# Kernel tuning notes

Hardware: AMD Instinct MI355X
Metric: run time of the kernel (lower is better)

Reference implementation:

```python
import jax, jax.numpy as jnp
import numpy as np

N_NODES = 50000
N_EDGES = 800000
MAX_ITER = 20  # torchdeq default f_max_iter=40; fixed iteration count for a tractable jit-able baseline
K = 3          # TAGConv default number of hops
INS, EMB, HID, OUT = 4, 64, 128, 1


def setup_inputs():
    key = jax.random.key(0)
    ks = jax.random.split(key, 12)
    def lin(k, fan_in, fan_out):
        return jax.random.normal(k, (fan_in, fan_out), jnp.float32) / np.sqrt(fan_in)
    def tag_w(k, fan_in, fan_out):
        # stacked weights for the K+1 TAGConv linear maps: [K+1, in, out]
        return jax.random.normal(k, (K + 1, fan_in, fan_out), jnp.float32) / np.sqrt(fan_in * (K + 1))
    return {
        "x": jax.random.normal(ks[0], (N_NODES, INS), jnp.float32),
        "pos": jax.random.normal(ks[1], (N_NODES, 3), jnp.float32),
        "edge_attr": jax.random.uniform(ks[2], (N_EDGES,), jnp.float32),
        "up_w1": lin(ks[3], INS, EMB), "up_b1": jnp.zeros((EMB,), jnp.float32),
        "up_w2": lin(ks[4], EMB, EMB), "up_b2": jnp.zeros((EMB,), jnp.float32),
        "c1_w": tag_w(ks[5], EMB + 3, HID), "c1_b": jnp.zeros((HID,), jnp.float32),
        "c2_w": tag_w(ks[6], HID, HID), "c2_b": jnp.zeros((HID,), jnp.float32),
        "c3_w": tag_w(ks[7], HID, EMB), "c3_b": jnp.zeros((EMB,), jnp.float32),
        "down_w1": lin(ks[8], EMB, OUT), "down_b1": jnp.zeros((OUT,), jnp.float32),
        "down_w2": lin(ks[9], OUT, OUT), "down_b2": jnp.zeros((OUT,), jnp.float32),
        "edge_index": jax.random.randint(ks[10], (2, N_EDGES), 0, N_NODES, jnp.int32),
    }


def _gcn_norm(row, col, edge_attr, n):
    # PyG gcn_norm with edge weights, no self loops (TAGConv default)
    deg = jax.ops.segment_sum(edge_attr, col, num_segments=n)
    safe = jnp.where(deg > 0, deg, 1.0)
    dinv = jnp.where(deg > 0, jax.lax.rsqrt(safe), 0.0)
    return dinv[row] * edge_attr * dinv[col]


def _mlp(x, w1, b1, w2, b2):
    # torch F.gelu default = exact erf gelu
    return jax.nn.gelu(x @ w1 + b1, approximate=False) @ w2 + b2


def reference(x, pos, edge_attr, up_w1, up_b1, up_w2, up_b2, c1_w, c1_b, c2_w, c2_b, c3_w, c3_b, down_w1, down_b1, down_w2, down_b2, edge_index):
    n = x.shape[0]
    row, col = edge_index[0], edge_index[1]
    norm = _gcn_norm(row, col, edge_attr, n)

    def tag(h, W, b):
        # TAGConv: sum_k lin_k( A_hat^k x ) + bias
        out = h @ W[0]
        for k in range(1, W.shape[0]):
            h = jax.ops.segment_sum(h[row] * norm[:, None], col, num_segments=n)  # [E,C] gather-scatter
            out = out + h @ W[k]
        return out + b

    def gnn(z):
        h = jnp.concatenate([z, pos], axis=1)
        h = jax.nn.relu(tag(h, c1_w, c1_b))
        h = jax.nn.relu(tag(h, c2_w, c2_b))  # F.dropout is identity in eval mode
        h = tag(h, c3_w, c3_b)
        return jax.nn.log_softmax(h, axis=1)

    z0 = _mlp(x, up_w1, up_b1, up_w2, up_b2)
    z = jax.lax.fori_loop(0, MAX_ITER, lambda i, zz: gnn(zz), z0)  # fixed-point solver
    z_star = gnn(z)  # phantom-gradient step (torchdeq grad=1)
    out = _mlp(z_star, down_w1, down_b1, down_w2, down_b2)
    return out, z_star
```

## Files before the change

kernel.cpp:

```cpp
#include <hip/hip_runtime.h>
#include <hip/hip_bf16.h>

#define N_NODES 50000
#define N_EDGES 800000
#define MAX_ITER 20

typedef __attribute__((ext_vector_type(8))) short bf16x8;
typedef __attribute__((ext_vector_type(4))) float f32x4;
typedef __attribute__((ext_vector_type(2))) float f32x2;
typedef unsigned char uchar;

__device__ __forceinline__ float gelu_f(float x){
  return 0.5f*x*(1.0f+erff(x*0.70710678118654752f));
}
__device__ __forceinline__ ushort f2b(float f){
  uint x = __float_as_uint(f);
  uint r = (x + 0x7fffu + ((x>>16)&1u)) >> 16;
  return (ushort)r;
}

#if __has_builtin(__builtin_amdgcn_cvt_pk_f32_fp8) && __has_builtin(__builtin_amdgcn_cvt_pk_fp8_f32)
#define HW_FP8 1
#endif

__device__ __forceinline__ uint fp8_enc1_sw(float x){
  uint u = __float_as_uint(x);
  uint s = (u>>24)&0x80u;
  int e = (int)((u>>23)&0xffu);
  uint m = u&0x7fffffu;
  uint m3 = (m + 0x80000u)>>20;
  if (m3==8u){ e+=1; m3=0u; }
  int e8 = e-120;
  if (e8<=0) return s;
  if (e8>=15) return s|0x7eu;
  return s | ((uint)e8<<3) | m3;
}
__device__ __forceinline__ float fp8_dec1_sw(uint b){
  uint s=(b&0x80u)<<24;
  uint em=b&0x7fu;
  if (em==0u) return __uint_as_float(s);
  if ((em>>3)==0u) return (s?-1.f:1.f)*(float)em*0.001953125f;
  return __uint_as_float(s | ((em+960u)<<20));
}
__device__ __forceinline__ void fp8_dec8(uint lo, uint hi, float* d){
#ifdef HW_FP8
  f32x2 a = __builtin_amdgcn_cvt_pk_f32_fp8(lo,false);
  f32x2 b = __builtin_amdgcn_cvt_pk_f32_fp8(lo,true);
  f32x2 c = __builtin_amdgcn_cvt_pk_f32_fp8(hi,false);
  f32x2 e = __builtin_amdgcn_cvt_pk_f32_fp8(hi,true);
  d[0]=a[0];d[1]=a[1];d[2]=b[0];d[3]=b[1];d[4]=c[0];d[5]=c[1];d[6]=e[0];d[7]=e[1];
#else
  d[0]=fp8_dec1_sw(lo&0xffu);        d[1]=fp8_dec1_sw((lo>>8)&0xffu);
  d[2]=fp8_dec1_sw((lo>>16)&0xffu);  d[3]=fp8_dec1_sw(lo>>24);
  d[4]=fp8_dec1_sw(hi&0xffu);        d[5]=fp8_dec1_sw((hi>>8)&0xffu);
  d[6]=fp8_dec1_sw((hi>>16)&0xffu);  d[7]=fp8_dec1_sw(hi>>24);
#endif
}
__device__ __forceinline__ uint fp8_enc4(float a,float b,float c,float d){
#ifdef HW_FP8
  uint u = __builtin_amdgcn_cvt_pk_fp8_f32(a,b,0u,false);
  u = __builtin_amdgcn_cvt_pk_fp8_f32(c,d,u,true);
  return u;
#else
  return fp8_enc1_sw(a) | (fp8_enc1_sw(b)<<8) | (fp8_enc1_sw(c)<<16) | (fp8_enc1_sw(d)<<24);
#endif
}
__device__ __forceinline__ uchar fp8_enc1(float a){
#ifdef HW_FP8
  return (uchar)(__builtin_amdgcn_cvt_pk_fp8_f32(a,a,0u,false)&0xffu);
#else
  return (uchar)fp8_enc1_sw(a);
#endif
}

__global__ void deg_cnt_kernel(const int* __restrict__ col, const float* __restrict__ attr,
                               float* __restrict__ deg, int* __restrict__ cnt){
  int e = blockIdx.x*256 + threadIdx.x;
  if (e < N_EDGES){
    int c = col[e];
    atomicAdd(&deg[c], attr[e]);
    atomicAdd(&cnt[c], 1);
  }
}

__global__ void norm_kernel(const int* __restrict__ row, const int* __restrict__ col,
                            const float* __restrict__ attr, const float* __restrict__ deg,
                            float* __restrict__ nrm){
  int e = blockIdx.x*256 + threadIdx.x;
  if (e < N_EDGES){
    float dr = deg[row[e]], dc = deg[col[e]];
    float ir = dr > 0.f ? rsqrtf(dr) : 0.f;
    float ic = dc > 0.f ? rsqrtf(dc) : 0.f;
    nrm[e] = ir * attr[e] * ic;
  }
}

__global__ void scan_kernel(const int* __restrict__ cnt, int* __restrict__ starts,
                            int* __restrict__ cursor){
  __shared__ int buf[1024];
  __shared__ int carry;
  int tid = threadIdx.x;
  if (tid==0) carry = 0;
  __syncthreads();
  for (int base=0; base<N_NODES; base+=1024){
    int i = base+tid;
    int v = (i<N_NODES)? cnt[i] : 0;
    int cv = carry;
    buf[tid]=v;
    __syncthreads();
    for (int off=1; off<1024; off<<=1){
      int t = (tid>=off)? buf[tid-off] : 0;
      __syncthreads();
      buf[tid]+=t;
      __syncthreads();
    }
    int excl = buf[tid]-v+cv;
    if (i<N_NODES){ starts[i]=excl; cursor[i]=excl; }
    __syncthreads();
    if (tid==0) carry = cv + buf[1023];
    __syncthreads();
  }
  if (tid==0) starts[N_NODES] = carry;
}

__global__ void fill_kernel(const int* __restrict__ row, const int* __restrict__ col,
                            const float* __restrict__ nrm, int* __restrict__ cursor,
                            int* __restrict__ csr_row, float* __restrict__ csr_nrm){
  int e = blockIdx.x*256+threadIdx.x;
  if (e<N_EDGES){
    int c = col[e];
    int p = atomicAdd(&cursor[c],1);
    csr_row[p]=row[e];
    csr_nrm[p]=nrm[e];
  }
}

__global__ void pack_w1(const float* __restrict__ W, ushort* __restrict__ PB){
  int i = blockIdx.x*256+threadIdx.x;
  if (i < 4*8*128*8){
    int e = i&7; int n = (i>>3)&127; int kb = (i>>10)&7; int j = i>>13;
    int k = kb*8+e;
    PB[i] = f2b(W[((size_t)j*67 + k)*128 + n]);
  }
}
__global__ void pack_w2(const float* __restrict__ W, ushort* __restrict__ PB){
  int i = blockIdx.x*256+threadIdx.x;
  if (i < 4*16*128*8){
    int e = i&7; int n = (i>>3)&127; int kb = (i>>10)&15; int j = i>>14;
    int k = kb*8+e;
    PB[i] = f2b(W[((size_t)j*128 + k)*128 + n]);
  }
}
__global__ void pack_w3(const float* __restrict__ W, ushort* __restrict__ PB){
  int i = blockIdx.x*256+threadIdx.x;
  if (i < 16*256*8){
    int e = i&7; int n = (i>>3)&255; int kb = i>>11;
    int k = kb*8+e;
    PB[i] = f2b(W[(((size_t)(n>>6))*128 + k)*64 + (n&63)]);
  }
}

__global__ __launch_bounds__(256) void mlp_up_kernel(
    const float* __restrict__ x, const float* __restrict__ w1, const float* __restrict__ b1,
    const float* __restrict__ w2, const float* __restrict__ b2,
    ushort* __restrict__ z, uchar* __restrict__ z8){
  __shared__ float sw1[4*64];
  __shared__ float sw2[64*64];
  __shared__ float sb1[64], sb2[64];
  __shared__ float t1s[4][64];
  int tid = threadIdx.x;
  for (int i=tid;i<256;i+=256) sw1[i]=w1[i];
  for (int i=tid;i<4096;i+=256) sw2[i]=w2[i];
  if (tid<64){ sb1[tid]=b1[tid]; sb2[tid]=b2[tid]; }
  __syncthreads();
  int g = tid>>6;
  int c = tid&63;
  int node = blockIdx.x*4 + g;
  float acc = sb1[c];
  #pragma unroll
  for (int k=0;k<4;k++) acc += x[node*4+k]*sw1[k*64+c];
  t1s[g][c] = gelu_f(acc);
  __syncthreads();
  float acc2 = sb2[c];
  #pragma unroll 8
  for (int k=0;k<64;k++) acc2 += t1s[g][k]*sw2[k*64+c];
  z[(size_t)node*64+c] = f2b(acc2);
  z8[(size_t)node*64+c] = fp8_enc1(acc2);
}

template<int LDIN>
__global__ void posprop(const float* __restrict__ in, float* __restrict__ out,
                        const int* __restrict__ starts, const int* __restrict__ crow,
                        const float* __restrict__ cnrm){
  int v = blockIdx.x*256+threadIdx.x;
  if (v >= N_NODES) return;
  int s=starts[v], e=starts[v+1];
  float a0=0.f,a1=0.f,a2=0.f;
  for (int i=s;i<e;++i){
    int r=crow[i]; float nm=cnrm[i];
    a0 = fmaf(in[(size_t)r*LDIN+0], nm, a0);
    a1 = fmaf(in[(size_t)r*LDIN+1], nm, a1);
    a2 = fmaf(in[(size_t)r*LDIN+2], nm, a2);
  }
  float4 o = {a0,a1,a2,0.f};
  *(float4*)(out + (size_t)v*4) = o;
}

__global__ __launch_bounds__(256) void posbias_kernel(
    const float* __restrict__ pos, const float* __restrict__ P1,
    const float* __restrict__ P2, const float* __restrict__ P3,
    const float* __restrict__ c1w, const float* __restrict__ c1b,
    ushort* __restrict__ pb){
  __shared__ float sw[4][3][128];
  int tid=threadIdx.x;
  for (int i=tid; i<4*3*128; i+=256){
    int cc=i&127; int d=(i>>7)%3; int j=i/(3*128);
    sw[j][d][cc] = c1w[((size_t)j*67 + 64 + d)*128 + cc];
  }
  __syncthreads();
  int idx = blockIdx.x*256+tid;
  if (idx < N_NODES*128){
    int n = idx>>7, cc = idx&127;
    float a = c1b[cc];
    #pragma unroll
    for (int d=0;d<3;d++) a = fmaf(pos[(size_t)n*3+d], sw[0][d][cc], a);
    #pragma unroll
    for (int d=0;d<3;d++) a = fmaf(P1[(size_t)n*4+d], sw[1][d][cc], a);
    #pragma unroll
    for (int d=0;d<3;d++) a = fmaf(P2[(size_t)n*4+d], sw[2][d][cc], a);
    #pragma unroll
    for (int d=0;d<3;d++) a = fmaf(P3[(size_t)n*4+d], sw[3][d][cc], a);
    pb[idx]=f2b(a);
  }
}

template<int MODE, bool IN8, bool OUT8>
__global__ __launch_bounds__(256) void prop64k(
    const void* __restrict__ hin, ushort* __restrict__ obf,
    uchar* __restrict__ of8, float* __restrict__ of32,
    const ushort* __restrict__ adj, const float* __restrict__ bias,
    const int* __restrict__ starts, const int* __restrict__ crow,
    const float* __restrict__ cnrm){
  constexpr bool WBF = (MODE==0) || (MODE==2) || (MODE==1 && !OUT8);
  int wv = threadIdx.x >> 6;
  int v = blockIdx.x*4 + wv;
  int t = threadIdx.x & 63;
  int g = t >> 3;
  int c = t & 7;
  int s = starts[v], e = starts[v+1];
  float acc[8] = {0,0,0,0,0,0,0,0};
  for (int i=s; i<e; i+=64){
    int cnt = e - i; if (cnt > 64) cnt = 64;
    int r = 0; float nm = 0.f;
    if (t < cnt){ r = crow[i+t]; nm = cnrm[i+t]; }
    for (int jb=0; jb<cnt; jb+=8){
      int rr = __shfl(r, jb+g, 64);
      float nmj = __shfl(nm, jb+g, 64);
      float hv[8];
      if (IN8){
        uint2 d = *(const uint2*)((const uchar*)hin + (size_t)rr*64 + c*8);
        fp8_dec8(d.x, d.y, hv);
      } else {
        uint4 d = *(const uint4*)((const ushort*)hin + (size_t)rr*64 + c*8);
        const uint* dp = (const uint*)&d;
        #pragma unroll
        for (int q=0;q<4;q++){
          hv[2*q]   = __uint_as_float(dp[q]<<16);
          hv[2*q+1] = __uint_as_float(dp[q]&0xffff0000u);
        }
      }
      #pragma unroll
      for (int q=0;q<8;q++) acc[q] = fmaf(hv[q], nmj, acc[q]);
    }
  }
  #pragma unroll
  for (int q=0;q<8;q++){
    acc[q] += __shfl_xor(acc[q], 8, 64);
    acc[q] += __shfl_xor(acc[q], 16, 64);
    acc[q] += __shfl_xor(acc[q], 32, 64);
  }
  if (MODE==0 || MODE==1){
    if (g==0){
      float val[8];
      if (MODE==1){
        uint4 av = *(const uint4*)(adj + (size_t)v*64 + c*8);
        const uint* ap=(const uint*)&av;
        #pragma unroll
        for (int q=0;q<4;q++){
          val[2*q]   = acc[2*q]   + __uint_as_float(ap[q]<<16);
          val[2*q+1] = acc[2*q+1] + __uint_as_float(ap[q]&0xffff0000u);
        }
      } else {
        #pragma unroll
        for (int q=0;q<8;q++) val[q]=acc[q];
      }
      if (WBF){
        uint4 o; uint* op=(uint*)&o;
        #pragma unroll
        for (int q=0;q<4;q++) op[q] = (uint)f2b(val[2*q]) | ((uint)f2b(val[2*q+1])<<16);
        *(uint4*)(obf + (size_t)v*64 + c*8) = o;
      }
      if (OUT8){
        uint2 o8;
        o8.x = fp8_enc4(val[0],val[1],val[2],val[3]);
        o8.y = fp8_enc4(val[4],val[5],val[6],val[7]);
        *(uint2*)(of8 + (size_t)v*64 + c*8) = o8;
      }
    }
  } else {
    uint4 av = *(const uint4*)(adj + (size_t)v*64 + c*8);
    const uint* ap=(const uint*)&av;
    float vv[8];
    #pragma unroll
    for (int q=0;q<4;q++){
      vv[2*q]   = acc[2*q]   + __uint_as_float(ap[q]<<16)         + bias[c*8+2*q];
      vv[2*q+1] = acc[2*q+1] + __uint_as_float(ap[q]&0xffff0000u) + bias[c*8+2*q+1];
    }
    float m = vv[0];
    #pragma unroll
    for (int q=1;q<8;q++) m = fmaxf(m, vv[q]);
    m = fmaxf(m, __shfl_xor(m,1,64));
    m = fmaxf(m, __shfl_xor(m,2,64));
    m = fmaxf(m, __shfl_xor(m,4,64));
    float ss = 0.f;
    #pragma unroll
    for (int q=0;q<8;q++) ss += __expf(vv[q]-m);
    ss += __shfl_xor(ss,1,64);
    ss += __shfl_xor(ss,2,64);
    ss += __shfl_xor(ss,4,64);
    float lse = m + __logf(ss);
    if (g==0){
      if (MODE==2){
        uint4 o; uint* op=(uint*)&o;
        #pragma unroll
        for (int q=0;q<4;q++) op[q] = (uint)f2b(vv[2*q]-lse) | ((uint)f2b(vv[2*q+1]-lse)<<16);
        *(uint4*)(obf + (size_t)v*64 + c*8) = o;
        if (OUT8){
          uint2 o8;
          o8.x = fp8_enc4(vv[0]-lse,vv[1]-lse,vv[2]-lse,vv[3]-lse);
          o8.y = fp8_enc4(vv[4]-lse,vv[5]-lse,vv[6]-lse,vv[7]-lse);
          *(uint2*)(of8 + (size_t)v*64 + c*8) = o8;
        }
      } else {
        float* zo = of32 + (size_t)v*64 + c*8;
        float4 o0 = {vv[0]-lse, vv[1]-lse, vv[2]-lse, vv[3]-lse};
        float4 o1 = {vv[4]-lse, vv[5]-lse, vv[6]-lse, vv[7]-lse};
        *(float4*)zo = o0;
        *(float4*)(zo+4) = o1;
      }
    }
  }
}

template<bool IN8, bool OUT8>
__global__ __launch_bounds__(256) void prop128k(
    const void* __restrict__ hin, ushort* __restrict__ obf,
    uchar* __restrict__ of8,
    const int* __restrict__ starts, const int* __restrict__ crow,
    const float* __restrict__ cnrm){
  int wv = threadIdx.x >> 6;
  int v = blockIdx.x*4 + wv;
  int t = threadIdx.x & 63;
  int g = t >> 4;
  int c = t & 15;
  int s = starts[v], e = starts[v+1];
  float acc[8] = {0,0,0,0,0,0,0,0};
  for (int i=s; i<e; i+=64){
    int cnt = e - i; if (cnt > 64) cnt = 64;
    int r = 0; float nm = 0.f;
    if (t < cnt){ r = crow[i+t]; nm = cnrm[i+t]; }
    for (int jb=0; jb<cnt; jb+=4){
      int rr  = __shfl(r,  jb+g, 64);
      float nmj = __shfl(nm, jb+g, 64);
      float hv[8];
      if (IN8){
        uint2 d = *(const uint2*)((const uchar*)hin + (size_t)rr*128 + c*8);
        fp8_dec8(d.x, d.y, hv);
      } else {
        uint4 d = *(const uint4*)((const ushort*)hin + (size_t)rr*128 + c*8);
        const uint* dp = (const uint*)&d;
        #pragma unroll
        for (int q=0;q<4;q++){
          hv[2*q]   = __uint_as_float(dp[q]<<16);
          hv[2*q+1] = __uint_as_float(dp[q]&0xffff0000u);
        }
      }
      #pragma unroll
      for (int q=0;q<8;q++) acc[q] = fmaf(hv[q], nmj, acc[q]);
    }
  }
  #pragma unroll
  for (int q=0;q<8;q++){
    acc[q] += __shfl_xor(acc[q], 16, 64);
    acc[q] += __shfl_xor(acc[q], 32, 64);
  }
  if (g==0){
    uint4 o; uint* op=(uint*)&o;
    #pragma unroll
    for (int q=0;q<4;q++) op[q] = (uint)f2b(acc[2*q]) | ((uint)f2b(acc[2*q+1])<<16);
    *(uint4*)(obf + (size_t)v*128 + c*8) = o;
    if (OUT8){
      uint2 o8;
      o8.x = fp8_enc4(acc[0],acc[1],acc[2],acc[3]);
      o8.y = fp8_enc4(acc[4],acc[5],acc[6],acc[7]);
      *(uint2*)(of8 + (size_t)v*128 + c*8) = o8;
    }
  }
}

template<int KC, bool PERNODE_BIAS, bool OUT8>
__global__ __launch_bounds__(256) void gemm4in(
    const ushort* __restrict__ H0, const ushort* __restrict__ H1,
    const ushort* __restrict__ H2, const ushort* __restrict__ H3,
    const ushort* __restrict__ PB, const void* __restrict__ biasp,
    ushort* __restrict__ out, uchar* __restrict__ out8){
  constexpr int NT = 8;
  constexpr int NKS = KC/32;
  int lane = threadIdx.x & 63;
  int wv   = threadIdx.x >> 6;
  int m0 = blockIdx.x*64 + wv*16;
  int lr = lane & 15, lg = lane >> 4;
  int arow = m0 + lr; if (arow > N_NODES-1) arow = N_NODES-1;
  const ushort* Hs[4] = {H0,H1,H2,H3};
  f32x4 acc[NT];
  #pragma unroll
  for (int t=0;t<NT;t++) acc[t] = (f32x4){0.f,0.f,0.f,0.f};
  #pragma unroll
  for (int j=0;j<4;j++){
    const ushort* Hj  = Hs[j] + (size_t)arow*KC + lg*8;
    const ushort* PBj = PB + (size_t)j*(KC/8)*128*8;
    #pragma unroll
    for (int ks=0; ks<NKS; ks++){
      bf16x8 af = *(const bf16x8*)(Hj + ks*32);
      int kb = ks*4 + lg;
      #pragma unroll
      for (int t=0;t<NT;t++){
        bf16x8 bf = *(const bf16x8*)(PBj + ((size_t)kb*128 + t*16 + lr)*8);
        acc[t] = __builtin_amdgcn_mfma_f32_16x16x32_bf16(af, bf, acc[t], 0, 0, 0);
      }
    }
  }
  #pragma unroll
  for (int t=0;t<NT;t++){
    #pragma unroll
    for (int q=0;q<4;q++){
      int node = m0 + lg*4 + q;
      if (node < N_NODES){
        int col = t*16 + lr;
        float b;
        if (PERNODE_BIAS) b = __uint_as_float(((uint)((const ushort*)biasp)[(size_t)node*128+col])<<16);
        else              b = ((const float*)biasp)[col];
        float vo = fmaxf(acc[t][q] + b, 0.f);
        out[(size_t)node*128 + col] = f2b(vo);
        if (OUT8) out8[(size_t)node*128 + col] = fp8_enc1(vo);
      }
    }
  }
}

__global__ __launch_bounds__(256) void gemm_y(
    const ushort* __restrict__ T2, const ushort* __restrict__ PB,
    ushort* __restrict__ Y, uchar* __restrict__ Y3_8){
  constexpr int NT = 16;
  int lane = threadIdx.x & 63;
  int wv   = threadIdx.x >> 6;
  int m0 = blockIdx.x*64 + wv*16;
  int lr = lane & 15, lg = lane >> 4;
  int arow = m0 + lr; if (arow > N_NODES-1) arow = N_NODES-1;
  f32x4 acc[NT];
  #pragma unroll
  for (int t=0;t<NT;t++) acc[t] = (f32x4){0.f,0.f,0.f,0.f};
  const ushort* Hj = T2 + (size_t)arow*128 + lg*8;
  #pragma unroll
  for (int ks=0; ks<4; ks++){
    bf16x8 af = *(const bf16x8*)(Hj + ks*32);
    int kb = ks*4 + lg;
    #pragma unroll
    for (int t=0;t<NT;t++){
      bf16x8 bf = *(const bf16x8*)(PB + ((size_t)kb*256 + t*16 + lr)*8);
      acc[t] = __builtin_amdgcn_mfma_f32_16x16x32_bf16(af, bf, acc[t], 0, 0, 0);
    }
  }
  #pragma unroll
  for (int t=0;t<NT;t++){
    int n = t*16 + lr;
    int j = n >> 6, cc = n & 63;
    #pragma unroll
    for (int q=0;q<4;q++){
      int node = m0 + lg*4 + q;
      if (node < N_NODES){
        Y[(size_t)j*N_NODES*64 + (size_t)node*64 + cc] = f2b(acc[t][q]);
        if (j==3) Y3_8[(size_t)node*64 + cc] = fp8_enc1(acc[t][q]);
      }
    }
  }
}

__global__ __launch_bounds__(256) void mlp_down_kernel(
    const float* __restrict__ zs, const float* __restrict__ dw1, const float* __restrict__ db1,
    const float* __restrict__ dw2, const float* __restrict__ db2, float* __restrict__ out){
  int node = blockIdx.x*4 + (threadIdx.x>>6);
  int c = threadIdx.x & 63;
  float v = zs[(size_t)node*64+c]*dw1[c];
  #pragma unroll
  for (int off=32; off; off>>=1) v += __shfl_xor(v, off, 64);
  if (c==0) out[node] = gelu_f(v + db1[0]) * dw2[0] + db2[0];
}

extern "C" void kernel_launch(void* const* d_in, const int* in_sizes, int n_in,
                              void* d_out, int out_size, void* d_ws, size_t ws_size,
                              hipStream_t stream){
  const float* x     = (const float*)d_in[0];
  const float* pos   = (const float*)d_in[1];
  const float* eattr = (const float*)d_in[2];
  const float* up_w1 = (const float*)d_in[3];
  const float* up_b1 = (const float*)d_in[4];
  const float* up_w2 = (const float*)d_in[5];
  const float* up_b2 = (const float*)d_in[6];
  const float* c1_w  = (const float*)d_in[7];
  const float* c1_b  = (const float*)d_in[8];
  const float* c2_w  = (const float*)d_in[9];
  const float* c2_b  = (const float*)d_in[10];
  const float* c3_w  = (const float*)d_in[11];
  const float* c3_b  = (const float*)d_in[12];
  const float* dw1   = (const float*)d_in[13];
  const float* db1   = (const float*)d_in[14];
  const float* dw2   = (const float*)d_in[15];
  const float* db2   = (const float*)d_in[16];
  const int*   eidx  = (const int*)d_in[17];
  const int* row = eidx;
  const int* col = eidx + N_EDGES;

  char* wsp = (char*)d_ws;
  size_t off = 0;
  auto alloc = [&](size_t bytes)->char*{
    char* p = wsp + off;
    off = (off + bytes + 255) & ~(size_t)255;
    return p;
  };
  float*  deg    = (float*)alloc((size_t)N_NODES*4);
  int*    cnt    = (int*)  alloc((size_t)N_NODES*4);
  int*    starts = (int*)  alloc((size_t)(N_NODES+1)*4);
  int*    cursor = (int*)  alloc((size_t)N_NODES*4);
  float*  nrm    = (float*)alloc((size_t)N_EDGES*4);
  int*    crow   = (int*)  alloc((size_t)N_EDGES*4);
  float*  cnrm   = (float*)alloc((size_t)N_EDGES*4);
  float*  P1     = (float*)alloc((size_t)N_NODES*4*4);
  float*  P2     = (float*)alloc((size_t)N_NODES*4*4);
  float*  P3     = (float*)alloc((size_t)N_NODES*4*4);
  ushort* pbias  = (ushort*)alloc((size_t)N_NODES*128*2);
  ushort* z      = (ushort*)alloc((size_t)N_NODES*64*2);
  ushort* q1     = (ushort*)alloc((size_t)N_NODES*64*2);
  ushort* q2     = (ushort*)alloc((size_t)N_NODES*64*2);
  ushort* q3     = (ushort*)alloc((size_t)N_NODES*64*2);
  ushort* t1     = (ushort*)alloc((size_t)N_NODES*128*2);
  ushort* p1     = (ushort*)alloc((size_t)N_NODES*128*2);
  ushort* p2     = (ushort*)alloc((size_t)N_NODES*128*2);
  ushort* p3     = (ushort*)alloc((size_t)N_NODES*128*2);
  ushort* t2     = (ushort*)alloc((size_t)N_NODES*128*2);
  ushort* PB1    = (ushort*)alloc((size_t)4*8*128*8*2);
  ushort* PB2    = (ushort*)alloc((size_t)4*16*128*8*2);
  ushort* PB3    = (ushort*)alloc((size_t)16*256*8*2);
  uchar*  z8     = (uchar*)alloc((size_t)N_NODES*64);
  uchar*  q1_8   = (uchar*)alloc((size_t)N_NODES*64);
  uchar*  q2_8   = (uchar*)alloc((size_t)N_NODES*64);
  uchar*  t1_8   = (uchar*)alloc((size_t)N_NODES*128);
  uchar*  p1_8   = (uchar*)alloc((size_t)N_NODES*128);
  uchar*  p2_8   = (uchar*)alloc((size_t)N_NODES*128);
  uchar*  Y3_8   = (uchar*)alloc((size_t)N_NODES*64);
  uchar*  u1_8   = (uchar*)alloc((size_t)N_NODES*64);
  uchar*  u2_8   = (uchar*)alloc((size_t)N_NODES*64);

  ushort* Y  = p1;
  ushort* Y0 = Y;
  ushort* Y1 = Y + (size_t)1*N_NODES*64;
  ushort* Y2 = Y + (size_t)2*N_NODES*64;
  ushort* Y3 = Y + (size_t)3*N_NODES*64;
  ushort* u1 = q1;
  ushort* u2 = q2;

  float* outv  = (float*)d_out;
  float* zstar = (float*)d_out + N_NODES;

  hipMemsetAsync(deg, 0, (size_t)N_NODES*4, stream);
  hipMemsetAsync(cnt, 0, (size_t)N_NODES*4, stream);
  int eb = (N_EDGES+255)/256;
  deg_cnt_kernel<<<eb,256,0,stream>>>(col, eattr, deg, cnt);
  norm_kernel<<<eb,256,0,stream>>>(row, col, eattr, deg, nrm);
  scan_kernel<<<1,1024,0,stream>>>(cnt, starts, cursor);
  fill_kernel<<<eb,256,0,stream>>>(row, col, nrm, cursor, crow, cnrm);
  pack_w1<<<128,256,0,stream>>>(c1_w, PB1);
  pack_w2<<<256,256,0,stream>>>(c2_w, PB2);
  pack_w3<<<128,256,0,stream>>>(c3_w, PB3);
  mlp_up_kernel<<<N_NODES/4,256,0,stream>>>(x, up_w1, up_b1, up_w2, up_b2, z, z8);

  int nb = (N_NODES+255)/256;
  posprop<3><<<nb,256,0,stream>>>(pos, P1, starts, crow, cnrm);
  posprop<4><<<nb,256,0,stream>>>(P1,  P2, starts, crow, cnrm);
  posprop<4><<<nb,256,0,stream>>>(P2,  P3, starts, crow, cnrm);
  posbias_kernel<<<(N_NODES*128)/256,256,0,stream>>>(pos, P1, P2, P3, c1_w, c1_b, pbias);

  const int gprop = N_NODES/4;
  const int ggemm = (N_NODES+63)/64;

  for (int it=0; it<=MAX_ITER; ++it){
    if (it < MAX_ITER){
      prop64k<0,true,true> <<<gprop,256,0,stream>>>(z8,   q1, q1_8, nullptr, nullptr, nullptr, starts, crow, cnrm);
      prop64k<0,true,true> <<<gprop,256,0,stream>>>(q1_8, q2, q2_8, nullptr, nullptr, nullptr, starts, crow, cnrm);
      prop64k<0,true,false><<<gprop,256,0,stream>>>(q2_8, q3, nullptr, nullptr, nullptr, nullptr, starts, crow, cnrm);
      gemm4in<64,true,true><<<ggemm,256,0,stream>>>(z,q1,q2,q3,PB1,pbias,t1,t1_8);

      prop128k<true,true> <<<gprop,256,0,stream>>>(t1_8, p1, p1_8, starts, crow, cnrm);
      prop128k<true,true> <<<gprop,256,0,stream>>>(p1_8, p2, p2_8, starts, crow, cnrm);
      prop128k<true,false><<<gprop,256,0,stream>>>(p2_8, p3, nullptr, starts, crow, cnrm);
      gemm4in<128,false,false><<<ggemm,256,0,stream>>>(t1,p1,p2,p3,PB2,c2_b,t2,nullptr);

      gemm_y<<<ggemm,256,0,stream>>>(t2, PB3, Y, Y3_8);
      prop64k<1,true,true><<<gprop,256,0,stream>>>(Y3_8, nullptr, u1_8, nullptr, Y2, nullptr, starts, crow, cnrm);
      prop64k<1,true,true><<<gprop,256,0,stream>>>(u1_8, nullptr, u2_8, nullptr, Y1, nullptr, starts, crow, cnrm);
      prop64k<2,true,true><<<gprop,256,0,stream>>>(u2_8, z, z8, nullptr, Y0, c3_b, starts, crow, cnrm);
    } else {
      prop64k<0,false,false><<<gprop,256,0,stream>>>(z,  q1, nullptr, nullptr, nullptr, nullptr, starts, crow, cnrm);
      prop64k<0,false,false><<<gprop,256,0,stream>>>(q1, q2, nullptr, nullptr, nullptr, nullptr, starts, crow, cnrm);
      prop64k<0,false,false><<<gprop,256,0,stream>>>(q2, q3, nullptr, nullptr, nullptr, nullptr, starts, crow, cnrm);
      gemm4in<64,true,false><<<ggemm,256,0,stream>>>(z,q1,q2,q3,PB1,pbias,t1,nullptr);

      prop128k<false,false><<<gprop,256,0,stream>>>(t1, p1, nullptr, starts, crow, cnrm);
      prop128k<false,false><<<gprop,256,0,stream>>>(p1, p2, nullptr, starts, crow, cnrm);
      prop128k<false,false><<<gprop,256,0,stream>>>(p2, p3, nullptr, starts, crow, cnrm);
      gemm4in<128,false,false><<<ggemm,256,0,stream>>>(t1,p1,p2,p3,PB2,c2_b,t2,nullptr);

      gemm_y<<<ggemm,256,0,stream>>>(t2, PB3, Y, Y3_8);
      prop64k<1,false,false><<<gprop,256,0,stream>>>(Y3, u1, nullptr, nullptr, Y2, nullptr, starts, crow, cnrm);
      prop64k<1,false,false><<<gprop,256,0,stream>>>(u1, u2, nullptr, nullptr, Y1, nullptr, starts, crow, cnrm);
      prop64k<3,false,false><<<gprop,256,0,stream>>>(u2, nullptr, nullptr, zstar, Y0, c3_b, starts, crow, cnrm);
    }
  }
  mlp_down_kernel<<<N_NODES/4,256,0,stream>>>(zstar, dw1, db1, dw2, db2, outv);
}
```

Baseline: 6.940 ms.

## Pack CSR row/norm into int2 and unroll gather loops with direct edge loads

Interleaves the CSR source index and edge weight into one 8-byte record, so each edge takes a single load instead of two separate arrays. The propagation kernels drop the load-to-registers plus shuffle broadcast. Each lane group now loads its own edge records directly with nontemporal loads and processes 2 (64-wide) or 4 (128-wide) edges per step, with clamped indices and zeroed weights for the tail. This aims to cut shuffle overhead and raise memory-level parallelism on the irregular gathers. The cost is redundant per-lane loads of the same edge record and more registers.

```diff
diff --git a/kernel.cpp b/kernel.cpp
--- a/kernel.cpp
+++ b/kernel.cpp
@@ -125,13 +125,12 @@
 
 __global__ void fill_kernel(const int* __restrict__ row, const int* __restrict__ col,
                             const float* __restrict__ nrm, int* __restrict__ cursor,
-                            int* __restrict__ csr_row, float* __restrict__ csr_nrm){
+                            int2* __restrict__ ep){
   int e = blockIdx.x*256+threadIdx.x;
   if (e<N_EDGES){
     int c = col[e];
     int p = atomicAdd(&cursor[c],1);
-    csr_row[p]=row[e];
-    csr_nrm[p]=nrm[e];
+    ep[p] = make_int2(row[e], __float_as_int(nrm[e]));
   }
 }
 
@@ -190,17 +189,17 @@
 
 template<int LDIN>
 __global__ void posprop(const float* __restrict__ in, float* __restrict__ out,
-                        const int* __restrict__ starts, const int* __restrict__ crow,
-                        const float* __restrict__ cnrm){
+                        const int* __restrict__ starts, const int2* __restrict__ ep){
   int v = blockIdx.x*256+threadIdx.x;
   if (v >= N_NODES) return;
   int s=starts[v], e=starts[v+1];
   float a0=0.f,a1=0.f,a2=0.f;
   for (int i=s;i<e;++i){
-    int r=crow[i]; float nm=cnrm[i];
-    a0 = fmaf(in[(size_t)r*LDIN+0], nm, a0);
-    a1 = fmaf(in[(size_t)r*LDIN+1], nm, a1);
-    a2 = fmaf(in[(size_t)r*LDIN+2], nm, a2);
+    int2 ed = ep[i];
+    float nm = __int_as_float(ed.y);
+    a0 = fmaf(in[(size_t)ed.x*LDIN+0], nm, a0);
+    a1 = fmaf(in[(size_t)ed.x*LDIN+1], nm, a1);
+    a2 = fmaf(in[(size_t)ed.x*LDIN+2], nm, a2);
   }
   float4 o = {a0,a1,a2,0.f};
   *(float4*)(out + (size_t)v*4) = o;
@@ -239,8 +238,7 @@
     const void* __restrict__ hin, ushort* __restrict__ obf,
     uchar* __restrict__ of8, float* __restrict__ of32,
     const ushort* __restrict__ adj, const float* __restrict__ bias,
-    const int* __restrict__ starts, const int* __restrict__ crow,
-    const float* __restrict__ cnrm){
+    const int* __restrict__ starts, const long long* __restrict__ ep){
   constexpr bool WBF = (MODE==0) || (MODE==2) || (MODE==1 && !OUT8);
   int wv = threadIdx.x >> 6;
   int v = blockIdx.x*4 + wv;
@@ -249,28 +247,36 @@
   int c = t & 7;
   int s = starts[v], e = starts[v+1];
   float acc[8] = {0,0,0,0,0,0,0,0};
-  for (int i=s; i<e; i+=64){
-    int cnt = e - i; if (cnt > 64) cnt = 64;
-    int r = 0; float nm = 0.f;
-    if (t < cnt){ r = crow[i+t]; nm = cnrm[i+t]; }
-    for (int jb=0; jb<cnt; jb+=8){
-      int rr = __shfl(r, jb+g, 64);
-      float nmj = __shfl(nm, jb+g, 64);
-      float hv[8];
-      if (IN8){
-        uint2 d = *(const uint2*)((const uchar*)hin + (size_t)rr*64 + c*8);
-        fp8_dec8(d.x, d.y, hv);
-      } else {
-        uint4 d = *(const uint4*)((const ushort*)hin + (size_t)rr*64 + c*8);
-        const uint* dp = (const uint*)&d;
-        #pragma unroll
-        for (int q=0;q<4;q++){
-          hv[2*q]   = __uint_as_float(dp[q]<<16);
-          hv[2*q+1] = __uint_as_float(dp[q]&0xffff0000u);
-        }
-      }
+  for (int i=s; i<e; i+=16){
+    int iA = i+g, iB = i+8+g;
+    int jA = min(iA, e-1), jB = min(iB, e-1);
+    long long pA = __builtin_nontemporal_load(ep+jA);
+    long long pB = __builtin_nontemporal_load(ep+jB);
+    float wA = (iA<e)? __int_as_float((int)(pA>>32)) : 0.f;
+    float wB = (iB<e)? __int_as_float((int)(pB>>32)) : 0.f;
+    int rA=(int)pA, rB=(int)pB;
+    float hvA[8], hvB[8];
+    if (IN8){
+      uint2 dA = *(const uint2*)((const uchar*)hin + (size_t)rA*64 + c*8);
+      uint2 dB = *(const uint2*)((const uchar*)hin + (size_t)rB*64 + c*8);
+      fp8_dec8(dA.x, dA.y, hvA);
+      fp8_dec8(dB.x, dB.y, hvB);
+    } else {
+      uint4 dA = *(const uint4*)((const ushort*)hin + (size_t)rA*64 + c*8);
+      uint4 dB = *(const uint4*)((const ushort*)hin + (size_t)rB*64 + c*8);
+      const uint* qA=(const uint*)&dA; const uint* qB=(const uint*)&dB;
       #pragma unroll
-      for (int q=0;q<8;q++) acc[q] = fmaf(hv[q], nmj, acc[q]);
+      for (int q=0;q<4;q++){
+        hvA[2*q]   = __uint_as_float(qA[q]<<16);
+        hvA[2*q+1] = __uint_as_float(qA[q]&0xffff0000u);
+        hvB[2*q]   = __uint_as_float(qB[q]<<16);
+        hvB[2*q+1] = __uint_as_float(qB[q]&0xffff0000u);
+      }
+    }
+    #pragma unroll
+    for (int q=0;q<8;q++){
+      acc[q] = fmaf(hvA[q], wA, acc[q]);
+      acc[q] = fmaf(hvB[q], wB, acc[q]);
     }
   }
   #pragma unroll
@@ -356,8 +362,7 @@
 __global__ __launch_bounds__(256) void prop128k(
     const void* __restrict__ hin, ushort* __restrict__ obf,
     uchar* __restrict__ of8,
-    const int* __restrict__ starts, const int* __restrict__ crow,
-    const float* __restrict__ cnrm){
+    const int* __restrict__ starts, const long long* __restrict__ ep){
   int wv = threadIdx.x >> 6;
   int v = blockIdx.x*4 + wv;
   int t = threadIdx.x & 63;
@@ -365,28 +370,47 @@
   int c = t & 15;
   int s = starts[v], e = starts[v+1];
   float acc[8] = {0,0,0,0,0,0,0,0};
-  for (int i=s; i<e; i+=64){
-    int cnt = e - i; if (cnt > 64) cnt = 64;
-    int r = 0; float nm = 0.f;
-    if (t < cnt){ r = crow[i+t]; nm = cnrm[i+t]; }
-    for (int jb=0; jb<cnt; jb+=4){
-      int rr  = __shfl(r,  jb+g, 64);
-      float nmj = __shfl(nm, jb+g, 64);
-      float hv[8];
-      if (IN8){
-        uint2 d = *(const uint2*)((const uchar*)hin + (size_t)rr*128 + c*8);
-        fp8_dec8(d.x, d.y, hv);
-      } else {
-        uint4 d = *(const uint4*)((const ushort*)hin + (size_t)rr*128 + c*8);
-        const uint* dp = (const uint*)&d;
-        #pragma unroll
-        for (int q=0;q<4;q++){
-          hv[2*q]   = __uint_as_float(dp[q]<<16);
-          hv[2*q+1] = __uint_as_float(dp[q]&0xffff0000u);
-        }
-      }
+  for (int i=s; i<e; i+=16){
+    int iA=i+g, iB=i+4+g, iC=i+8+g, iD=i+12+g;
+    int jA=min(iA,e-1), jB=min(iB,e-1), jC=min(iC,e-1), jD=min(iD,e-1);
+    long long pA = __builtin_nontemporal_load(ep+jA);
+    long long pB = __builtin_nontemporal_load(ep+jB);
+    long long pC = __builtin_nontemporal_load(ep+jC);
+    long long pD = __builtin_nontemporal_load(ep+jD);
+    float wA=(iA<e)?__int_as_float((int)(pA>>32)):0.f;
+    float wB=(iB<e)?__int_as_float((int)(pB>>32)):0.f;
+    float wC=(iC<e)?__int_as_float((int)(pC>>32)):0.f;
+    float wD=(iD<e)?__int_as_float((int)(pD>>32)):0.f;
+    int rA=(int)pA, rB=(int)pB, rC=(int)pC, rD=(int)pD;
+    float hvA[8], hvB[8], hvC[8], hvD[8];
+    if (IN8){
+      uint2 dA = *(const uint2*)((const uchar*)hin + (size_t)rA*128 + c*8);
+      uint2 dB = *(const uint2*)((const uchar*)hin + (size_t)rB*128 + c*8);
+      uint2 dC = *(const uint2*)((const uchar*)hin + (size_t)rC*128 + c*8);
+      uint2 dD = *(const uint2*)((const uchar*)hin + (size_t)rD*128 + c*8);
+      fp8_dec8(dA.x,dA.y,hvA); fp8_dec8(dB.x,dB.y,hvB);
+      fp8_dec8(dC.x,dC.y,hvC); fp8_dec8(dD.x,dD.y,hvD);
+    } else {
+      uint4 dA = *(const uint4*)((const ushort*)hin + (size_t)rA*128 + c*8);
+      uint4 dB = *(const uint4*)((const ushort*)hin + (size_t)rB*128 + c*8);
+      uint4 dC = *(const uint4*)((const ushort*)hin + (size_t)rC*128 + c*8);
+      uint4 dD = *(const uint4*)((const ushort*)hin + (size_t)rD*128 + c*8);
+      const uint* qA=(const uint*)&dA; const uint* qB=(const uint*)&dB;
+      const uint* qC=(const uint*)&dC; const uint* qD=(const uint*)&dD;
       #pragma unroll
-      for (int q=0;q<8;q++) acc[q] = fmaf(hv[q], nmj, acc[q]);
+      for (int q=0;q<4;q++){
+        hvA[2*q]=__uint_as_float(qA[q]<<16); hvA[2*q+1]=__uint_as_float(qA[q]&0xffff0000u);
+        hvB[2*q]=__uint_as_float(qB[q]<<16); hvB[2*q+1]=__uint_as_float(qB[q]&0xffff0000u);
+        hvC[2*q]=__uint_as_float(qC[q]<<16); hvC[2*q+1]=__uint_as_float(qC[q]&0xffff0000u);
+        hvD[2*q]=__uint_as_float(qD[q]<<16); hvD[2*q+1]=__uint_as_float(qD[q]&0xffff0000u);
+      }
+    }
+    #pragma unroll
+    for (int q=0;q<8;q++){
+      acc[q] = fmaf(hvA[q], wA, acc[q]);
+      acc[q] = fmaf(hvB[q], wB, acc[q]);
+      acc[q] = fmaf(hvC[q], wC, acc[q]);
+      acc[q] = fmaf(hvD[q], wD, acc[q]);
     }
   }
   #pragma unroll
@@ -543,8 +567,7 @@
   int*    starts = (int*)  alloc((size_t)(N_NODES+1)*4);
   int*    cursor = (int*)  alloc((size_t)N_NODES*4);
   float*  nrm    = (float*)alloc((size_t)N_EDGES*4);
-  int*    crow   = (int*)  alloc((size_t)N_EDGES*4);
-  float*  cnrm   = (float*)alloc((size_t)N_EDGES*4);
+  int2*   ep     = (int2*) alloc((size_t)N_EDGES*8);
   float*  P1     = (float*)alloc((size_t)N_NODES*4*4);
   float*  P2     = (float*)alloc((size_t)N_NODES*4*4);
   float*  P3     = (float*)alloc((size_t)N_NODES*4*4);
@@ -582,22 +605,24 @@
   float* outv  = (float*)d_out;
   float* zstar = (float*)d_out + N_NODES;
 
+  const long long* epl = (const long long*)ep;
+
   hipMemsetAsync(deg, 0, (size_t)N_NODES*4, stream);
   hipMemsetAsync(cnt, 0, (size_t)N_NODES*4, stream);
   int eb = (N_EDGES+255)/256;
   deg_cnt_kernel<<<eb,256,0,stream>>>(col, eattr, deg, cnt);
   norm_kernel<<<eb,256,0,stream>>>(row, col, eattr, deg, nrm);
   scan_kernel<<<1,1024,0,stream>>>(cnt, starts, cursor);
-  fill_kernel<<<eb,256,0,stream>>>(row, col, nrm, cursor, crow, cnrm);
+  fill_kernel<<<eb,256,0,stream>>>(row, col, nrm, cursor, ep);
   pack_w1<<<128,256,0,stream>>>(c1_w, PB1);
   pack_w2<<<256,256,0,stream>>>(c2_w, PB2);
   pack_w3<<<128,256,0,stream>>>(c3_w, PB3);
   mlp_up_kernel<<<N_NODES/4,256,0,stream>>>(x, up_w1, up_b1, up_w2, up_b2, z, z8);
 
   int nb = (N_NODES+255)/256;
-  posprop<3><<<nb,256,0,stream>>>(pos, P1, starts, crow, cnrm);
-  posprop<4><<<nb,256,0,stream>>>(P1,  P2, starts, crow, cnrm);
-  posprop<4><<<nb,256,0,stream>>>(P2,  P3, starts, crow, cnrm);
+  posprop<3><<<nb,256,0,stream>>>(pos, P1, starts, ep);
+  posprop<4><<<nb,256,0,stream>>>(P1,  P2, starts, ep);
+  posprop<4><<<nb,256,0,stream>>>(P2,  P3, starts, ep);
   posbias_kernel<<<(N_NODES*128)/256,256,0,stream>>>(pos, P1, P2, P3, c1_w, c1_b, pbias);
 
   const int gprop = N_NODES/4;
@@ -605,35 +630,35 @@
 
   for (int it=0; it<=MAX_ITER; ++it){
     if (it < MAX_ITER){
-      prop64k<0,true,true> <<<gprop,256,0,stream>>>(z8,   q1, q1_8, nullptr, nullptr, nullptr, starts, crow, cnrm);
-      prop64k<0,true,true> <<<gprop,256,0,stream>>>(q1_8, q2, q2_8, nullptr, nullptr, nullptr, starts, crow, cnrm);
-      prop64k<0,true,false><<<gprop,256,0,stream>>>(q2_8, q3, nullptr, nullptr, nullptr, nullptr, starts, crow, cnrm);
+      prop64k<0,true,true> <<<gprop,256,0,stream>>>(z8,   q1, q1_8, nullptr, nullptr, nullptr, starts, epl);
+      prop64k<0,true,true> <<<gprop,256,0,stream>>>(q1_8, q2, q2_8, nullptr, nullptr, nullptr, starts, epl);
+      prop64k<0,true,false><<<gprop,256,0,stream>>>(q2_8, q3, nullptr, nullptr, nullptr, nullptr, starts, epl);
       gemm4in<64,true,true><<<ggemm,256,0,stream>>>(z,q1,q2,q3,PB1,pbias,t1,t1_8);
 
-      prop128k<true,true> <<<gprop,256,0,stream>>>(t1_8, p1, p1_8, starts, crow, cnrm);
-      prop128k<true,true> <<<gprop,256,0,stream>>>(p1_8, p2, p2_8, starts, crow, cnrm);
-      prop128k<true,false><<<gprop,256,0,stream>>>(p2_8, p3, nullptr, starts, crow, cnrm);
+      prop128k<true,true> <<<gprop,256,0,stream>>>(t1_8, p1, p1_8, starts, epl);
+      prop128k<true,true> <<<gprop,256,0,stream>>>(p1_8, p2, p2_8, starts, epl);
+      prop128k<true,false><<<gprop,256,0,stream>>>(p2_8, p3, nullptr, starts, epl);
       gemm4in<128,false,false><<<ggemm,256,0,stream>>>(t1,p1,p2,p3,PB2,c2_b,t2,nullptr);
 
       gemm_y<<<ggemm,256,0,stream>>>(t2, PB3, Y, Y3_8);
-      prop64k<1,true,true><<<gprop,256,0,stream>>>(Y3_8, nullptr, u1_8, nullptr, Y2, nullptr, starts, crow, cnrm);
-      prop64k<1,true,true><<<gprop,256,0,stream>>>(u1_8, nullptr, u2_8, nullptr, Y1, nullptr, starts, crow, cnrm);
-      prop64k<2,true,true><<<gprop,256,0,stream>>>(u2_8, z, z8, nullptr, Y0, c3_b, starts, crow, cnrm);
+      prop64k<1,true,true><<<gprop,256,0,stream>>>(Y3_8, nullptr, u1_8, nullptr, Y2, nullptr, starts, epl);
+      prop64k<1,true,true><<<gprop,256,0,stream>>>(u1_8, nullptr, u2_8, nullptr, Y1, nullptr, starts, epl);
+      prop64k<2,true,true><<<gprop,256,0,stream>>>(u2_8, z, z8, nullptr, Y0, c3_b, starts, epl);
     } else {
-      prop64k<0,false,false><<<gprop,256,0,stream>>>(z,  q1, nullptr, nullptr, nullptr, nullptr, starts, crow, cnrm);
-      prop64k<0,false,false><<<gprop,256,0,stream>>>(q1, q2, nullptr, nullptr, nullptr, nullptr, starts, crow, cnrm);
-      prop64k<0,false,false><<<gprop,256,0,stream>>>(q2, q3, nullptr, nullptr, nullptr, nullptr, starts, crow, cnrm);
+      prop64k<0,false,false><<<gprop,256,0,stream>>>(z,  q1, nullptr, nullptr, nullptr, nullptr, starts, epl);
+      prop64k<0,false,false><<<gprop,256,0,stream>>>(q1, q2, nullptr, nullptr, nullptr, nullptr, starts, epl);
+      prop64k<0,false,false><<<gprop,256,0,stream>>>(q2, q3, nullptr, nullptr, nullptr, nullptr, starts, epl);
       gemm4in<64,true,false><<<ggemm,256,0,stream>>>(z,q1,q2,q3,PB1,pbias,t1,nullptr);
 
-      prop128k<false,false><<<gprop,256,0,stream>>>(t1, p1, nullptr, starts, crow, cnrm);
-      prop128k<false,false><<<gprop,256,0,stream>>>(p1, p2, nullptr, starts, crow, cnrm);
-      prop128k<false,false><<<gprop,256,0,stream>>>(p2, p3, nullptr, starts, crow, cnrm);
+      prop128k<false,false><<<gprop,256,0,stream>>>(t1, p1, nullptr, starts, epl);
+      prop128k<false,false><<<gprop,256,0,stream>>>(p1, p2, nullptr, starts, epl);
+      prop128k<false,false><<<gprop,256,0,stream>>>(p2, p3, nullptr, starts, epl);
       gemm4in<128,false,false><<<ggemm,256,0,stream>>>(t1,p1,p2,p3,PB2,c2_b,t2,nullptr);
 
       gemm_y<<<ggemm,256,0,stream>>>(t2, PB3, Y, Y3_8);
-      prop64k<1,false,false><<<gprop,256,0,stream>>>(Y3, u1, nullptr, nullptr, Y2, nullptr, starts, crow, cnrm);
-      prop64k<1,false,false><<<gprop,256,0,stream>>>(u1, u2, nullptr, nullptr, Y1, nullptr, starts, crow, cnrm);
-      prop64k<3,false,false><<<gprop,256,0,stream>>>(u2, nullptr, nullptr, zstar, Y0, c3_b, starts, crow, cnrm);
+      prop64k<1,false,false><<<gprop,256,0,stream>>>(Y3, u1, nullptr, nullptr, Y2, nullptr, starts, epl);
+      prop64k<1,false,false><<<gprop,256,0,stream>>>(u1, u2, nullptr, nullptr, Y1, nullptr, starts, epl);
+      prop64k<3,false,false><<<gprop,256,0,stream>>>(u2, nullptr, nullptr, zstar, Y0, c3_b, starts, epl);
     }
   }
   mlp_down_kernel<<<N_NODES/4,256,0,stream>>>(zstar, dw1, db1, dw2, db2, outv);
```

After: 7.255 ms. +4.5%, slower.
